# Optimization experiments

Hardware: AMD Instinct MI355X
Metric: run time of the kernel (lower is better)

The kernel has to match this reference:

```python
import jax, jax.numpy as jnp
import numpy as np
import math

B, S, D, H = 2, 2048, 1024, 16
DK = D // H


def setup_inputs() -> dict:
    key = jax.random.key(0)
    ks = jax.random.split(key, 8)
    s = 1.0 / math.sqrt(D)
    inp = {
        "query": jax.random.normal(ks[0], (B, S, D), jnp.float32),
        "key": jax.random.normal(ks[1], (B, S, D), jnp.float32),
        "value": jax.random.normal(ks[2], (B, S, D), jnp.float32),
        # causal mask: (1, 1, S, S), 1 where attention allowed
        "mask": jnp.tril(jnp.ones((S, S), jnp.int32))[None, None, :, :],
        "Wq": jax.random.normal(ks[3], (D, D), jnp.float32) * s,
        "Wk": jax.random.normal(ks[4], (D, D), jnp.float32) * s,
        "Wv": jax.random.normal(ks[5], (D, D), jnp.float32) * s,
        "Wo": jax.random.normal(ks[6], (D, D), jnp.float32) * s,
    }
    return inp


def reference(query, key, value, mask, Wq, Wk, Wv, Wo):
    # nn.Linear(bias=False): y = x @ W.T
    def proj_heads(x, W):
        y = jnp.einsum("bsd,ed->bse", x, W)          # (B,S,D)
        return y.reshape(B, -1, H, DK).transpose(0, 2, 1, 3)  # (B,H,S,DK)

    q = proj_heads(query, Wq)
    k = proj_heads(key, Wk)
    v = proj_heads(value, Wv)

    scale = jnp.asarray(math.sqrt(DK), q.dtype)
    scores = jnp.einsum("bhqd,bhkd->bhqk", q, k) / scale  # (B,H,S,S)
    scores = jnp.where(mask == 0, -jnp.inf, scores)
    attn = jax.nn.softmax(scores, axis=-1)
    # dropout p=0.0 (eval): identity
    out = jnp.einsum("bhqk,bhkd->bhqd", attn, v)          # (B,H,S,DK)
    concat = out.transpose(0, 2, 1, 3).reshape(B, -1, D)  # (B,S,D)
    return jnp.einsum("bsd,ed->bse", concat, Wo)
```

## Files before the change

### kernel.cpp

```cpp
#include <hip/hip_runtime.h>
#include <hip/hip_bf16.h>

#define B_ 2
#define S_ 2048
#define D_ 1024
#define H_ 16
#define DK_ 64

typedef __hip_bfloat16 bf16;
typedef __attribute__((ext_vector_type(8))) short bf16x8;
typedef __attribute__((ext_vector_type(4))) short bf16x4;
typedef __attribute__((ext_vector_type(4))) float f32x4;

#define GLDS16(g, l)                                                     \
    __builtin_amdgcn_global_load_lds(                                    \
        (const __attribute__((address_space(1))) void*)(g),              \
        (__attribute__((address_space(3))) void*)(l), 16, 0, 0)

#define MFMA_K32(a, b, c) __builtin_amdgcn_mfma_f32_16x16x32_bf16(a, b, c, 0, 0, 0)
#define MFMA_K16(a, b, c) __builtin_amdgcn_mfma_f32_16x16x16bf16_1k(a, b, c, 0, 0, 0)
#define EXP2F(x) __builtin_amdgcn_exp2f(x)

__global__ __launch_bounds__(256) void cvt_all(
    const float* __restrict__ q, const float* __restrict__ k, const float* __restrict__ v,
    const float* __restrict__ w0, const float* __restrict__ w1,
    const float* __restrict__ w2, const float* __restrict__ w3,
    bf16* __restrict__ oq, bf16* __restrict__ ok, bf16* __restrict__ ov,
    bf16* __restrict__ o0, bf16* __restrict__ o1, bf16* __restrict__ o2,
    bf16* __restrict__ o3) {
    int bid = blockIdx.x;
    const float* src; bf16* dst; int base;
    if      (bid < 2048) { src = q;  dst = oq; base = bid; }
    else if (bid < 4096) { src = k;  dst = ok; base = bid - 2048; }
    else if (bid < 6144) { src = v;  dst = ov; base = bid - 4096; }
    else if (bid < 6656) { src = w0; dst = o0; base = bid - 6144; }
    else if (bid < 7168) { src = w1; dst = o1; base = bid - 6656; }
    else if (bid < 7680) { src = w2; dst = o2; base = bid - 7168; }
    else                 { src = w3; dst = o3; base = bid - 7680; }
    int i = (base * 256 + threadIdx.x) * 8;
    float4 a = *(const float4*)(src + i);
    float4 b = *(const float4*)(src + i + 4);
    __align__(16) bf16 o[8];
    o[0] = __float2bfloat16(a.x); o[1] = __float2bfloat16(a.y);
    o[2] = __float2bfloat16(a.z); o[3] = __float2bfloat16(a.w);
    o[4] = __float2bfloat16(b.x); o[5] = __float2bfloat16(b.y);
    o[6] = __float2bfloat16(b.z); o[7] = __float2bfloat16(b.w);
    *(bf16x8*)(dst + i) = *(const bf16x8*)o;
}

__device__ __forceinline__ void proj_loop(const bf16* __restrict__ X,
                                          const bf16* __restrict__ W,
                                          int m0, int n0, bf16* As, bf16* Bs,
                                          f32x4 (&acc)[2][8]) {
    const int K = D_;
    const int tid = threadIdx.x;
    const int lane = tid & 63, wave = tid >> 6;
    const int lm = lane & 15, quad = lane >> 4;

    auto stage = [&](int t, int bf) {
        int k0 = t * 32;
        bf16* Ab = As + bf * (128 * 32);
        bf16* Bb = Bs + bf * (128 * 32);
#pragma unroll
        for (int i = 0; i < 2; ++i) {
            int s = i * 256 + tid;
            int row = s >> 2;
            int c = (s & 3) ^ ((row >> 1) & 3);
            GLDS16(X + (size_t)(m0 + row) * K + k0 + c * 8, Ab + s * 8);
        }
#pragma unroll
        for (int i = 0; i < 2; ++i) {
            int s = i * 256 + tid;
            int row = s >> 2;
            int c = (s & 3) ^ ((row >> 1) & 3);
            GLDS16(W + (size_t)(n0 + row) * K + k0 + c * 8, Bb + s * 8);
        }
    };

    stage(0, 0);
    for (int t = 0; t < K / 32; ++t) {
        __syncthreads();
        if (t + 1 < K / 32) stage(t + 1, (t + 1) & 1);
        const bf16* Ab = As + (t & 1) * (128 * 32);
        const bf16* Bb = Bs + (t & 1) * (128 * 32);
        bf16x8 aF[2], bF[8];
#pragma unroll
        for (int mt = 0; mt < 2; ++mt) {
            int row = wave * 32 + mt * 16 + lm;
            aF[mt] = *(const bf16x8*)(Ab + row * 32 + (quad ^ ((row >> 1) & 3)) * 8);
        }
#pragma unroll
        for (int nt = 0; nt < 8; ++nt) {
            int row = nt * 16 + lm;
            bF[nt] = *(const bf16x8*)(Bb + row * 32 + (quad ^ ((row >> 1) & 3)) * 8);
        }
#pragma unroll
        for (int mt = 0; mt < 2; ++mt)
#pragma unroll
            for (int nt = 0; nt < 8; ++nt)
                acc[mt][nt] = MFMA_K32(aF[mt], bF[nt], acc[mt][nt]);
    }
}

__global__ __launch_bounds__(256) void proj_qkv(
    const bf16* __restrict__ qx, const bf16* __restrict__ kx, const bf16* __restrict__ vx,
    const bf16* __restrict__ wq, const bf16* __restrict__ wk, const bf16* __restrict__ wv,
    bf16* __restrict__ qb, bf16* __restrict__ kb, bf16* __restrict__ vtb) {
    __shared__ __align__(16) bf16 As[2 * 128 * 32];
    __shared__ __align__(16) bf16 Bs[2 * 128 * 32];
    const int z = blockIdx.z;
    const bf16* X = (z == 0) ? qx : (z == 1) ? kx : vx;
    const bf16* W = (z == 0) ? wq : (z == 1) ? wk : wv;
    const int n0 = blockIdx.x * 128;
    const int m0 = blockIdx.y * 128;
    f32x4 acc[2][8] = {};
    proj_loop(X, W, m0, n0, As, Bs, acc);

    const int lane = threadIdx.x & 63, wave = threadIdx.x >> 6;
    const int lm = lane & 15, quad = lane >> 4;
#pragma unroll
    for (int mt = 0; mt < 2; ++mt) {
        int mbase = m0 + wave * 32 + mt * 16 + quad * 4;
#pragma unroll
        for (int nt = 0; nt < 8; ++nt) {
            int n = n0 + nt * 16 + lm;
            if (z == 2) {
                int b = mbase >> 11, s = mbase & (S_ - 1);
                unsigned short u[4];
#pragma unroll
                for (int r = 0; r < 4; ++r) {
                    bf16 hv = __float2bfloat16(acc[mt][nt][r]);
                    u[r] = *(unsigned short*)&hv;
                }
                ushort4 pk = {u[0], u[1], u[2], u[3]};
                *(ushort4*)(vtb + ((size_t)(b * 1024 + n) * S_ + s)) = pk;
            } else {
                bf16* Y = z ? kb : qb;
#pragma unroll
                for (int r = 0; r < 4; ++r)
                    Y[(size_t)(mbase + r) * D_ + n] = __float2bfloat16(acc[mt][nt][r]);
            }
        }
    }
}

__global__ __launch_bounds__(256) void proj_o(const bf16* __restrict__ X,
                                              const bf16* __restrict__ W,
                                              float* __restrict__ Y) {
    __shared__ __align__(16) bf16 As[2 * 128 * 32];
    __shared__ __align__(16) bf16 Bs[2 * 128 * 32];
    const int n0 = blockIdx.x * 128;
    const int m0 = blockIdx.y * 128;
    f32x4 acc[2][8] = {};
    proj_loop(X, W, m0, n0, As, Bs, acc);

    const int lane = threadIdx.x & 63, wave = threadIdx.x >> 6;
    const int lm = lane & 15, quad = lane >> 4;
#pragma unroll
    for (int mt = 0; mt < 2; ++mt) {
        int mbase = m0 + wave * 32 + mt * 16 + quad * 4;
#pragma unroll
        for (int nt = 0; nt < 8; ++nt) {
            int n = n0 + nt * 16 + lm;
#pragma unroll
            for (int r = 0; r < 4; ++r)
                Y[(size_t)(mbase + r) * D_ + n] = acc[mt][nt][r];
        }
    }
}

__global__ __launch_bounds__(256) void attn_kernel(const bf16* __restrict__ Q,
                                                   const bf16* __restrict__ Kb,
                                                   const bf16* __restrict__ VT,
                                                   bf16* __restrict__ O) {
    __shared__ __align__(16) bf16 kt[2][128 * 64];
    __shared__ __align__(16) bf16 vt[2][64 * 128];

    const int tid = threadIdx.x;
    const int lane = tid & 63, wave = tid >> 6;
    const int lm = lane & 15, quad = lane >> 4;
    const int qc = (int)(gridDim.x - 1 - blockIdx.x);
    const int h = blockIdx.y, b = blockIdx.z;
    const int q0 = qc * 128 + wave * 32;

    const size_t bhoff = (size_t)b * S_ * D_ + (size_t)h * DK_;
    const bf16* vtb = VT + ((size_t)b * 1024 + h * DK_) * S_;

    bf16x8 aq[2][2];
#pragma unroll
    for (int mt = 0; mt < 2; ++mt) {
        const bf16* qp = Q + bhoff + (size_t)(q0 + mt * 16 + lm) * D_ + quad * 8;
        aq[mt][0] = *(const bf16x8*)(qp);
        aq[mt][1] = *(const bf16x8*)(qp + 32);
    }

    f32x4 oacc[2][4] = {};
    float lsum[2] = {0.f, 0.f};
    const float cexp = 0.125f * 1.44269504f;

    const int trips = qc + 1;

    auto stage = [&](int i, int bf) {
        int j0s = i * 128;
#pragma unroll
        for (int ii = 0; ii < 4; ++ii) {
            int s = ii * 256 + tid;
            int j = s >> 3, c = (s & 7) ^ (j & 7);
            GLDS16(Kb + bhoff + (size_t)(j0s + j) * D_ + c * 8, kt[bf] + s * 8);
        }
#pragma unroll
        for (int ii = 0; ii < 4; ++ii) {
            int s = ii * 256 + tid;
            int d = s >> 4, c = (s & 15) ^ (d & 15);
            GLDS16(vtb + (size_t)d * S_ + j0s + c * 8, vt[bf] + s * 8);
        }
    };

    stage(0, 0);

    for (int i = 0; i < trips; ++i) {
        __syncthreads();
        if (i + 1 < trips) stage(i + 1, (i + 1) & 1);
        const int j0 = i * 128;
        if (j0 > q0 + 31) continue;
        const bf16* ktb = kt[i & 1];
        const bf16* vtl = vt[i & 1];

#pragma unroll
        for (int st = 0; st < 8; ++st) {
            const int jc = j0 + st * 16;
            if (jc > q0 + 31) break;
            int j = st * 16 + lm;
            bf16x8 bk0 = *(const bf16x8*)(ktb + (((j << 3) | (quad ^ (j & 7))) * 8));
            bf16x8 bk1 = *(const bf16x8*)(ktb + (((j << 3) | ((4 + quad) ^ (j & 7))) * 8));

            const bool act0 = (jc <= q0 + 15);
            bf16x4 pa[2];
#pragma unroll
            for (int mt = 0; mt < 2; ++mt) {
                if (mt == 0 && !act0) continue;
                const int q0m = q0 + mt * 16;
                f32x4 z = {};
                z = MFMA_K32(bk0, aq[mt][0], z);
                z = MFMA_K32(bk1, aq[mt][1], z);
                const bool mk = (jc + 15 > q0m);
                const int qrow = q0m + lm;
                float rs = 0.f;
#pragma unroll
                for (int r = 0; r < 4; ++r) {
                    float p = EXP2F(z[r] * cexp);
                    if (mk && (jc + quad * 4 + r > qrow)) p = 0.f;
                    z[r] = p;
                    rs += p;
                }
                lsum[mt] += rs;
#pragma unroll
                for (int r = 0; r < 4; ++r) {
                    bf16 hv = __float2bfloat16(z[r]);
                    pa[mt][r] = *(short*)&hv;
                }
            }

#pragma unroll
            for (int dt = 0; dt < 4; ++dt) {
                int d = dt * 16 + lm;
                int cl = st * 2 + (quad >> 1);
                const bf16* vp = vtl + d * 128 + ((cl ^ (d & 15)) * 8 + (quad & 1) * 4);
                bf16x4 bv = *(const bf16x4*)vp;
                if (act0) oacc[0][dt] = MFMA_K16(pa[0], bv, oacc[0][dt]);
                oacc[1][dt] = MFMA_K16(pa[1], bv, oacc[1][dt]);
            }
        }
    }

#pragma unroll
    for (int mt = 0; mt < 2; ++mt) {
        float l = lsum[mt];
        l += __shfl_xor(l, 16, 64);
        l += __shfl_xor(l, 32, 64);
#pragma unroll
        for (int r = 0; r < 4; ++r) {
            float inv = 1.f / __shfl(l, quad * 4 + r, 64);
            int qrow = q0 + mt * 16 + quad * 4 + r;
#pragma unroll
            for (int dt = 0; dt < 4; ++dt) {
                int d = dt * 16 + lm;
                O[bhoff + (size_t)qrow * D_ + d] = __float2bfloat16(oacc[mt][dt][r] * inv);
            }
        }
    }
}

extern "C" void kernel_launch(void* const* d_in, const int* in_sizes, int n_in,
                              void* d_out, int out_size, void* d_ws, size_t ws_size,
                              hipStream_t stream) {
    const float* q_in = (const float*)d_in[0];
    const float* k_in = (const float*)d_in[1];
    const float* v_in = (const float*)d_in[2];
    const float* Wq_f = (const float*)d_in[4];
    const float* Wk_f = (const float*)d_in[5];
    const float* Wv_f = (const float*)d_in[6];
    const float* Wo_f = (const float*)d_in[7];
    float* out = (float*)d_out;

    const size_t NEL = (size_t)B_ * S_ * D_;
    const size_t WEL = (size_t)D_ * D_;
    bf16* p = (bf16*)d_ws;
    bf16* qx = p;  p += NEL;
    bf16* kx = p;  p += NEL;
    bf16* vx = p;  p += NEL;
    bf16* wq = p;  p += WEL;
    bf16* wk = p;  p += WEL;
    bf16* wv = p;  p += WEL;
    bf16* wo = p;  p += WEL;
    bf16* qb = p;  p += NEL;
    bf16* kb = p;  p += NEL;
    bf16* vtb = p; p += NEL;
    bf16* cb = p;  p += NEL;

    cvt_all<<<8192, 256, 0, stream>>>(q_in, k_in, v_in, Wq_f, Wk_f, Wv_f, Wo_f,
                                      qx, kx, vx, wq, wk, wv, wo);

    dim3 gqkv(D_ / 128, (B_ * S_) / 128, 3);
    proj_qkv<<<gqkv, 256, 0, stream>>>(qx, kx, vx, wq, wk, wv, qb, kb, vtb);

    dim3 gattn(S_ / 128, H_, B_);
    attn_kernel<<<gattn, 256, 0, stream>>>(qb, kb, vtb, cb);

    dim3 gproj(D_ / 128, (B_ * S_) / 128);
    proj_o<<<gproj, 256, 0, stream>>>(cb, wo, out);
}
```

Measured before the change: 261.7 us.

## Use 8 waves per attention block and narrower output-projection tiles

The attention kernel now runs 512 threads per 128-row query block, with each wave owning 16 query rows instead of 32. This halves per-wave accumulator state and gives the causal diagonal tile a cleaner per-wave chunk schedule. The output projection is templated to use 128x64 tiles, doubling its grid to fill more compute units. The costs are more blocks, more redundant A-tile loads in the projection, and fewer registers available per thread in attention.

Result: faster. 238.5 us (-8.9%).

```diff
diff --git a/kernel.cpp b/kernel.cpp
--- a/kernel.cpp
+++ b/kernel.cpp
@@ -48,19 +48,21 @@
     *(bf16x8*)(dst + i) = *(const bf16x8*)o;
 }
 
+template <int NT>
 __device__ __forceinline__ void proj_loop(const bf16* __restrict__ X,
                                           const bf16* __restrict__ W,
                                           int m0, int n0, bf16* As, bf16* Bs,
-                                          f32x4 (&acc)[2][8]) {
+                                          f32x4 (&acc)[2][NT]) {
     const int K = D_;
     const int tid = threadIdx.x;
     const int lane = tid & 63, wave = tid >> 6;
     const int lm = lane & 15, quad = lane >> 4;
+    constexpr int BROWS = NT * 16;
 
     auto stage = [&](int t, int bf) {
         int k0 = t * 32;
         bf16* Ab = As + bf * (128 * 32);
-        bf16* Bb = Bs + bf * (128 * 32);
+        bf16* Bb = Bs + bf * (BROWS * 32);
 #pragma unroll
         for (int i = 0; i < 2; ++i) {
             int s = i * 256 + tid;
@@ -69,7 +71,7 @@
             GLDS16(X + (size_t)(m0 + row) * K + k0 + c * 8, Ab + s * 8);
         }
 #pragma unroll
-        for (int i = 0; i < 2; ++i) {
+        for (int i = 0; i < NT / 4; ++i) {
             int s = i * 256 + tid;
             int row = s >> 2;
             int c = (s & 3) ^ ((row >> 1) & 3);
@@ -82,22 +84,22 @@
         __syncthreads();
         if (t + 1 < K / 32) stage(t + 1, (t + 1) & 1);
         const bf16* Ab = As + (t & 1) * (128 * 32);
-        const bf16* Bb = Bs + (t & 1) * (128 * 32);
-        bf16x8 aF[2], bF[8];
+        const bf16* Bb = Bs + (t & 1) * (BROWS * 32);
+        bf16x8 aF[2], bF[NT];
 #pragma unroll
         for (int mt = 0; mt < 2; ++mt) {
             int row = wave * 32 + mt * 16 + lm;
             aF[mt] = *(const bf16x8*)(Ab + row * 32 + (quad ^ ((row >> 1) & 3)) * 8);
         }
 #pragma unroll
-        for (int nt = 0; nt < 8; ++nt) {
+        for (int nt = 0; nt < NT; ++nt) {
             int row = nt * 16 + lm;
             bF[nt] = *(const bf16x8*)(Bb + row * 32 + (quad ^ ((row >> 1) & 3)) * 8);
         }
 #pragma unroll
         for (int mt = 0; mt < 2; ++mt)
 #pragma unroll
-            for (int nt = 0; nt < 8; ++nt)
+            for (int nt = 0; nt < NT; ++nt)
                 acc[mt][nt] = MFMA_K32(aF[mt], bF[nt], acc[mt][nt]);
     }
 }
@@ -114,7 +116,7 @@
     const int n0 = blockIdx.x * 128;
     const int m0 = blockIdx.y * 128;
     f32x4 acc[2][8] = {};
-    proj_loop(X, W, m0, n0, As, Bs, acc);
+    proj_loop<8>(X, W, m0, n0, As, Bs, acc);
 
     const int lane = threadIdx.x & 63, wave = threadIdx.x >> 6;
     const int lm = lane & 15, quad = lane >> 4;
@@ -148,11 +150,11 @@
                                               const bf16* __restrict__ W,
                                               float* __restrict__ Y) {
     __shared__ __align__(16) bf16 As[2 * 128 * 32];
-    __shared__ __align__(16) bf16 Bs[2 * 128 * 32];
-    const int n0 = blockIdx.x * 128;
+    __shared__ __align__(16) bf16 Bs[2 * 64 * 32];
+    const int n0 = blockIdx.x * 64;
     const int m0 = blockIdx.y * 128;
-    f32x4 acc[2][8] = {};
-    proj_loop(X, W, m0, n0, As, Bs, acc);
+    f32x4 acc[2][4] = {};
+    proj_loop<4>(X, W, m0, n0, As, Bs, acc);
 
     const int lane = threadIdx.x & 63, wave = threadIdx.x >> 6;
     const int lm = lane & 15, quad = lane >> 4;
@@ -160,7 +162,7 @@
     for (int mt = 0; mt < 2; ++mt) {
         int mbase = m0 + wave * 32 + mt * 16 + quad * 4;
 #pragma unroll
-        for (int nt = 0; nt < 8; ++nt) {
+        for (int nt = 0; nt < 4; ++nt) {
             int n = n0 + nt * 16 + lm;
 #pragma unroll
             for (int r = 0; r < 4; ++r)
@@ -169,7 +171,7 @@
     }
 }
 
-__global__ __launch_bounds__(256) void attn_kernel(const bf16* __restrict__ Q,
+__global__ __launch_bounds__(512) void attn_kernel(const bf16* __restrict__ Q,
                                                    const bf16* __restrict__ Kb,
                                                    const bf16* __restrict__ VT,
                                                    bf16* __restrict__ O) {
@@ -181,112 +183,90 @@
     const int lm = lane & 15, quad = lane >> 4;
     const int qc = (int)(gridDim.x - 1 - blockIdx.x);
     const int h = blockIdx.y, b = blockIdx.z;
-    const int q0 = qc * 128 + wave * 32;
+    const int q0 = qc * 128 + wave * 16;
 
     const size_t bhoff = (size_t)b * S_ * D_ + (size_t)h * DK_;
     const bf16* vtb = VT + ((size_t)b * 1024 + h * DK_) * S_;
 
-    bf16x8 aq[2][2];
-#pragma unroll
-    for (int mt = 0; mt < 2; ++mt) {
-        const bf16* qp = Q + bhoff + (size_t)(q0 + mt * 16 + lm) * D_ + quad * 8;
-        aq[mt][0] = *(const bf16x8*)(qp);
-        aq[mt][1] = *(const bf16x8*)(qp + 32);
-    }
-
-    f32x4 oacc[2][4] = {};
-    float lsum[2] = {0.f, 0.f};
+    const bf16* qp = Q + bhoff + (size_t)(q0 + lm) * D_ + quad * 8;
+    bf16x8 aq0 = *(const bf16x8*)(qp);
+    bf16x8 aq1 = *(const bf16x8*)(qp + 32);
+
+    f32x4 oacc[4] = {};
+    float lsum = 0.f;
     const float cexp = 0.125f * 1.44269504f;
-
-    const int trips = qc + 1;
 
     auto stage = [&](int i, int bf) {
         int j0s = i * 128;
 #pragma unroll
-        for (int ii = 0; ii < 4; ++ii) {
-            int s = ii * 256 + tid;
+        for (int ii = 0; ii < 2; ++ii) {
+            int s = ii * 512 + tid;
             int j = s >> 3, c = (s & 7) ^ (j & 7);
             GLDS16(Kb + bhoff + (size_t)(j0s + j) * D_ + c * 8, kt[bf] + s * 8);
         }
 #pragma unroll
-        for (int ii = 0; ii < 4; ++ii) {
-            int s = ii * 256 + tid;
+        for (int ii = 0; ii < 2; ++ii) {
+            int s = ii * 512 + tid;
             int d = s >> 4, c = (s & 15) ^ (d & 15);
             GLDS16(vtb + (size_t)d * S_ + j0s + c * 8, vt[bf] + s * 8);
         }
     };
 
+    auto chunk = [&](const bf16* ktb, const bf16* vtl, int st, bool mk) {
+        int j = st * 16 + lm;
+        bf16x8 bk0 = *(const bf16x8*)(ktb + (((j << 3) | (quad ^ (j & 7))) * 8));
+        bf16x8 bk1 = *(const bf16x8*)(ktb + (((j << 3) | ((4 + quad) ^ (j & 7))) * 8));
+        f32x4 z = {};
+        z = MFMA_K32(bk0, aq0, z);
+        z = MFMA_K32(bk1, aq1, z);
+        bf16x4 pa;
+        float rs = 0.f;
+#pragma unroll
+        for (int r = 0; r < 4; ++r) {
+            float p = EXP2F(z[r] * cexp);
+            if (mk && (quad * 4 + r > lm)) p = 0.f;
+            rs += p;
+            bf16 hv = __float2bfloat16(p);
+            pa[r] = *(short*)&hv;
+        }
+        lsum += rs;
+#pragma unroll
+        for (int dt = 0; dt < 4; ++dt) {
+            int d = dt * 16 + lm;
+            int cl = st * 2 + (quad >> 1);
+            bf16x4 bv = *(const bf16x4*)(vtl + d * 128 +
+                                         ((cl ^ (d & 15)) * 8 + (quad & 1) * 4));
+            oacc[dt] = MFMA_K16(pa, bv, oacc[dt]);
+        }
+    };
+
     stage(0, 0);
 
-    for (int i = 0; i < trips; ++i) {
+    for (int i = 0; i <= qc; ++i) {
         __syncthreads();
-        if (i + 1 < trips) stage(i + 1, (i + 1) & 1);
-        const int j0 = i * 128;
-        if (j0 > q0 + 31) continue;
+        if (i < qc) stage(i + 1, (i + 1) & 1);
         const bf16* ktb = kt[i & 1];
         const bf16* vtl = vt[i & 1];
-
-#pragma unroll
-        for (int st = 0; st < 8; ++st) {
-            const int jc = j0 + st * 16;
-            if (jc > q0 + 31) break;
-            int j = st * 16 + lm;
-            bf16x8 bk0 = *(const bf16x8*)(ktb + (((j << 3) | (quad ^ (j & 7))) * 8));
-            bf16x8 bk1 = *(const bf16x8*)(ktb + (((j << 3) | ((4 + quad) ^ (j & 7))) * 8));
-
-            const bool act0 = (jc <= q0 + 15);
-            bf16x4 pa[2];
-#pragma unroll
-            for (int mt = 0; mt < 2; ++mt) {
-                if (mt == 0 && !act0) continue;
-                const int q0m = q0 + mt * 16;
-                f32x4 z = {};
-                z = MFMA_K32(bk0, aq[mt][0], z);
-                z = MFMA_K32(bk1, aq[mt][1], z);
-                const bool mk = (jc + 15 > q0m);
-                const int qrow = q0m + lm;
-                float rs = 0.f;
-#pragma unroll
-                for (int r = 0; r < 4; ++r) {
-                    float p = EXP2F(z[r] * cexp);
-                    if (mk && (jc + quad * 4 + r > qrow)) p = 0.f;
-                    z[r] = p;
-                    rs += p;
-                }
-                lsum[mt] += rs;
-#pragma unroll
-                for (int r = 0; r < 4; ++r) {
-                    bf16 hv = __float2bfloat16(z[r]);
-                    pa[mt][r] = *(short*)&hv;
-                }
-            }
-
-#pragma unroll
-            for (int dt = 0; dt < 4; ++dt) {
-                int d = dt * 16 + lm;
-                int cl = st * 2 + (quad >> 1);
-                const bf16* vp = vtl + d * 128 + ((cl ^ (d & 15)) * 8 + (quad & 1) * 4);
-                bf16x4 bv = *(const bf16x4*)vp;
-                if (act0) oacc[0][dt] = MFMA_K16(pa[0], bv, oacc[0][dt]);
-                oacc[1][dt] = MFMA_K16(pa[1], bv, oacc[1][dt]);
-            }
-        }
-    }
-
-#pragma unroll
-    for (int mt = 0; mt < 2; ++mt) {
-        float l = lsum[mt];
-        l += __shfl_xor(l, 16, 64);
-        l += __shfl_xor(l, 32, 64);
-#pragma unroll
-        for (int r = 0; r < 4; ++r) {
-            float inv = 1.f / __shfl(l, quad * 4 + r, 64);
-            int qrow = q0 + mt * 16 + quad * 4 + r;
-#pragma unroll
-            for (int dt = 0; dt < 4; ++dt) {
-                int d = dt * 16 + lm;
-                O[bhoff + (size_t)qrow * D_ + d] = __float2bfloat16(oacc[mt][dt][r] * inv);
-            }
+        if (i < qc) {
+#pragma unroll
+            for (int st = 0; st < 8; ++st) chunk(ktb, vtl, st, false);
+        } else {
+            for (int st = 0; st < wave; ++st) chunk(ktb, vtl, st, false);
+            chunk(ktb, vtl, wave, true);
+        }
+    }
+
+    float l = lsum;
+    l += __shfl_xor(l, 16, 64);
+    l += __shfl_xor(l, 32, 64);
+#pragma unroll
+    for (int r = 0; r < 4; ++r) {
+        float inv = 1.f / __shfl(l, quad * 4 + r, 64);
+        int qrow = q0 + quad * 4 + r;
+#pragma unroll
+        for (int dt = 0; dt < 4; ++dt) {
+            int d = dt * 16 + lm;
+            O[bhoff + (size_t)qrow * D_ + d] = __float2bfloat16(oacc[dt][r] * inv);
         }
     }
 }
@@ -325,8 +305,8 @@
     proj_qkv<<<gqkv, 256, 0, stream>>>(qx, kx, vx, wq, wk, wv, qb, kb, vtb);
 
     dim3 gattn(S_ / 128, H_, B_);
-    attn_kernel<<<gattn, 256, 0, stream>>>(qb, kb, vtb, cb);
-
-    dim3 gproj(D_ / 128, (B_ * S_) / 128);
+    attn_kernel<<<gattn, 512, 0, stream>>>(qb, kb, vtb, cb);
+
+    dim3 gproj(D_ / 64, (B_ * S_) / 128);
     proj_o<<<gproj, 256, 0, stream>>>(cb, wo, out);
 }
```
